# Optimization experiments

Measured on AMD Instinct MI355X. Metric: run time of the kernel, lower is better.

The kernel has to match this reference:

```python
import jax, jax.numpy as jnp
import numpy as np

B, NPTS, T, P, C, D = 2, 32768, 32768, 512, 4, 768


def _sincos_pos_embed(centers, embed_dim):
    # centers: np [P,3]; matches get_3d_sincos_pos_embed
    c = centers - centers.mean(axis=0)
    c = c / np.linalg.norm(c, axis=1).max()
    div = np.exp(np.arange(0, embed_dim, 6) * -(np.log(10000.0) / embed_dim))  # [D/6]
    arg = c[:, None, :] * div[None, :, None]                                   # [P, D/6, 3]
    pe = np.concatenate([np.sin(arg), np.cos(arg)], axis=-1).reshape(centers.shape[0], embed_dim)
    return pe.astype(np.float32)


def setup_inputs() -> dict:
    key = jax.random.key(0)
    ks = jax.random.split(key, 12)
    rng = np.random.default_rng(0)

    # ragged patch sizes (avg 64) summing exactly to T
    sizes = rng.integers(32, 97, size=P).astype(np.int64)
    sizes = np.maximum((sizes * (T / sizes.sum())).astype(np.int64), 1)
    sizes[-1] += T - sizes.sum()
    patch_offset = jnp.asarray(np.concatenate([[0], np.cumsum(sizes)]), dtype=jnp.int32)  # [P+1]

    patch_index = jax.random.randint(ks[0], (T,), 0, NPTS, dtype=jnp.int32)
    latent = jax.random.normal(ks[1], (B, NPTS, C), dtype=jnp.float32)

    s = 0.02
    params = dict(
        w1a=jax.random.normal(ks[2], (C, D), jnp.float32) * s,
        b1a=jnp.zeros((D,), jnp.float32),
        w1b=jax.random.normal(ks[3], (D, D), jnp.float32) * s,
        b1b=jnp.zeros((D,), jnp.float32),
        w2a=jax.random.normal(ks[4], (2 * D, D), jnp.float32) * s,
        b2a=jnp.zeros((D,), jnp.float32),
        g2=jnp.ones((D,), jnp.float32),
        beta2=jnp.zeros((D,), jnp.float32),
        w2b=jax.random.normal(ks[5], (D, D), jnp.float32) * s,
        b2b=jnp.zeros((D,), jnp.float32),
    )

    centers = rng.standard_normal((P, 3))
    pos_embed = jnp.asarray(_sincos_pos_embed(centers, D))[None]  # [1, P, D]

    return dict(latent=latent, patch_index=patch_index, patch_offset=patch_offset,
                pos_embed=pos_embed, **params)


def _ln(x, eps, gamma=None, beta=None):
    mu = x.mean(axis=-1, keepdims=True)
    var = ((x - mu) ** 2).mean(axis=-1, keepdims=True)
    y = (x - mu) * jax.lax.rsqrt(var + eps)
    if gamma is not None:
        y = y * gamma + beta
    return y


def reference(latent, patch_index, patch_offset, pos_embed,
              w1a, b1a, w1b, b1b, w2a, b2a, g2, beta2, w2b, b2b):
    T_ = patch_index.shape[0]
    P_ = patch_offset.shape[0] - 1
    # segment id of each token (repeat_interleave inverse): seg[t] = patch containing t
    seg = jnp.searchsorted(patch_offset[1:], jnp.arange(T_, dtype=patch_offset.dtype), side='right')

    x = latent[:, patch_index, :]                           # [B, T, C] gather
    h = x @ w1a + b1a
    h = jax.nn.gelu(_ln(h, 1e-6), approximate=False)
    h = h @ w1b + b1b                                       # [B, T, D]

    segmax = lambda a: jax.ops.segment_max(a, seg, num_segments=P_)
    y = jax.vmap(segmax)(h)                                 # [B, P, D] ragged max-pool

    h2 = jnp.concatenate([y[:, seg, :], h], axis=-1)        # repeat_interleave + concat
    h2 = h2 @ w2a + b2a
    h2 = jax.nn.gelu(_ln(h2, 1e-5, g2, beta2), approximate=False)
    h2 = h2 @ w2b + b2b                                     # [B, T, D]
    raw_latent = h2

    out = jax.vmap(segmax)(raw_latent) + pos_embed          # [B, P, D]
    return out.astype(raw_latent.dtype), raw_latent
```

## Files before the change

### kernel.cpp

```cpp
#include <hip/hip_runtime.h>
#include <hip/hip_bf16.h>
#include <math.h>

#define B_    2
#define NPTS_ 32768
#define T_    32768
#define P_    512
#define C_    4
#define D_    768
#define M_    (B_ * T_)

typedef __bf16 bf16_t;
typedef __bf16 bf16x8 __attribute__((ext_vector_type(8)));
typedef __bf16 bf16x4 __attribute__((ext_vector_type(4)));
typedef float  f32x4  __attribute__((ext_vector_type(4)));

__device__ inline void gload16(const void* g, void* l) {
  __builtin_amdgcn_global_load_lds(
      (const __attribute__((address_space(1))) void*)g,
      (__attribute__((address_space(3))) void*)l, 16, 0, 0);
}

__device__ inline float gelu_exact(float x) {
  return 0.5f * x * (1.0f + erff(x * 0.70710678118654752f));
}

__device__ inline unsigned fmap(float x) {
  unsigned u = __float_as_uint(x);
  return (u & 0x80000000u) ? ~u : (u | 0x80000000u);
}
__device__ inline float funmap(unsigned u) {
  unsigned v = (u & 0x80000000u) ? (u & 0x7FFFFFFFu) : ~u;
  return __uint_as_float(v);
}

__global__ __launch_bounds__(256) void prep_kernel(
    const int* __restrict__ off, int* __restrict__ seg, uint4* __restrict__ umax,
    const float* __restrict__ w1b, const float* __restrict__ w2a,
    const float* __restrict__ w2b,
    bf16_t* __restrict__ w1bT, bf16_t* __restrict__ w2aTT,
    bf16_t* __restrict__ w2aBT, bf16_t* __restrict__ w2bT) {
  __shared__ float tile[32][33];
  int bid = blockIdx.x, tid = threadIdx.x;
  if (bid < 2304) {
    const float* src; bf16_t* dst;
    int which = bid / 576, r = bid - which * 576;
    if (which == 0)      { src = w1b;             dst = w1bT;  }
    else if (which == 1) { src = w2a;             dst = w2aTT; }
    else if (which == 2) { src = w2a + D_ * D_;   dst = w2aBT; }
    else                 { src = w2b;             dst = w2bT;  }
    int n0 = (r % 24) * 32, k0 = (r / 24) * 32;
    int tx = tid & 31, ty = tid >> 5;
    #pragma unroll
    for (int i = 0; i < 4; ++i)
      tile[ty + 8 * i][tx] = src[(size_t)(k0 + ty + 8 * i) * D_ + n0 + tx];
    __syncthreads();
    #pragma unroll
    for (int i = 0; i < 4; ++i)
      dst[(size_t)(n0 + ty + 8 * i) * D_ + k0 + tx] = (bf16_t)tile[tx][ty + 8 * i];
  } else if (bid < 2432) {
    int t = (bid - 2304) * 256 + tid;
    int lo = 0, hi = P_;
    while (lo < hi) {
      int mid = (lo + hi) >> 1;
      if (off[mid + 1] <= t) lo = mid + 1; else hi = mid;
    }
    seg[t] = lo;
  } else {
    umax[(size_t)(bid - 2432) * 256 + tid] = make_uint4(0, 0, 0, 0);
  }
}

__global__ __launch_bounds__(256) void yconv_kernel(
    const uint4* __restrict__ ymax, bf16_t* __restrict__ y) {
  int t = blockIdx.x * 256 + threadIdx.x;
  uint4 u = ymax[t];
  bf16x4 o;
  o[0] = (bf16_t)funmap(u.x); o[1] = (bf16_t)funmap(u.y);
  o[2] = (bf16_t)funmap(u.z); o[3] = (bf16_t)funmap(u.w);
  *(bf16x4*)(y + (size_t)t * 4) = o;
}

__global__ __launch_bounds__(256) void final2_kernel(
    const uint4* __restrict__ rmax, const float4* __restrict__ pe,
    float4* __restrict__ out) {
  int t = blockIdx.x * 256 + threadIdx.x;
  int row = t / 192, col = t % 192;
  uint4 u = rmax[t];
  float4 p = pe[(row & (P_ - 1)) * 192 + col];
  float4 o;
  o.x = funmap(u.x) + p.x; o.y = funmap(u.y) + p.y;
  o.z = funmap(u.z) + p.z; o.w = funmap(u.w) + p.w;
  out[t] = o;
}

__global__ __launch_bounds__(256) void embed_kernel(
    const float4* __restrict__ latent4, const int* __restrict__ pidx,
    const float* __restrict__ w1a, const float* __restrict__ b1a,
    bf16_t* __restrict__ act1) {
  int wid = threadIdx.x >> 6, lane = threadIdx.x & 63;
  int m = blockIdx.x * 4 + wid;
  int b = m >> 15, t = m & (T_ - 1);
  float4 x = latent4[(size_t)b * NPTS_ + pidx[t]];
  int d8 = lane * 8, d4 = 512 + lane * 4;
  float v[12];
  {
    float4 a0 = *(const float4*)(b1a + d8);
    float4 a1 = *(const float4*)(b1a + d8 + 4);
    float4 a2 = *(const float4*)(b1a + d4);
    v[0]=a0.x; v[1]=a0.y; v[2]=a0.z; v[3]=a0.w;
    v[4]=a1.x; v[5]=a1.y; v[6]=a1.z; v[7]=a1.w;
    v[8]=a2.x; v[9]=a2.y; v[10]=a2.z; v[11]=a2.w;
  }
  float xk[4] = {x.x, x.y, x.z, x.w};
  #pragma unroll
  for (int k = 0; k < 4; ++k) {
    const float* w = w1a + k * D_;
    float4 w0 = *(const float4*)(w + d8);
    float4 w1 = *(const float4*)(w + d8 + 4);
    float4 w2 = *(const float4*)(w + d4);
    float f = xk[k];
    v[0] += f*w0.x; v[1] += f*w0.y; v[2] += f*w0.z; v[3] += f*w0.w;
    v[4] += f*w1.x; v[5] += f*w1.y; v[6] += f*w1.z; v[7] += f*w1.w;
    v[8] += f*w2.x; v[9] += f*w2.y; v[10]+= f*w2.z; v[11]+= f*w2.w;
  }
  float sum = 0.f, sq = 0.f;
  #pragma unroll
  for (int j = 0; j < 12; ++j) { sum += v[j]; sq += v[j]*v[j]; }
  #pragma unroll
  for (int o = 32; o > 0; o >>= 1) { sum += __shfl_xor(sum, o); sq += __shfl_xor(sq, o); }
  float mu = sum * (1.0f / D_);
  float rstd = rsqrtf(sq * (1.0f / D_) - mu * mu + 1e-6f);
  bf16x8 o8; bf16x4 o4;
  #pragma unroll
  for (int j = 0; j < 8; ++j) o8[j] = (bf16_t)gelu_exact((v[j] - mu) * rstd);
  #pragma unroll
  for (int j = 0; j < 4; ++j) o4[j] = (bf16_t)gelu_exact((v[8 + j] - mu) * rstd);
  size_t base = (size_t)m * D_;
  *(bf16x8*)(act1 + base + d8) = o8;
  *(bf16x4*)(act1 + base + d4) = o4;
}

__global__ __launch_bounds__(256) void ln2_kernel(
    const bf16_t* __restrict__ h2pre, const float* __restrict__ z,
    const int* __restrict__ seg, const float* __restrict__ g2,
    const float* __restrict__ beta2, bf16_t* __restrict__ act2) {
  int wid = threadIdx.x >> 6, lane = threadIdx.x & 63;
  int m = blockIdx.x * 4 + wid;
  int b = m >> 15, t = m & (T_ - 1);
  int d8 = lane * 8, d4 = 512 + lane * 4;
  size_t base = (size_t)m * D_;
  const float* zrow = z + (size_t)((b << 9) + seg[t]) * D_;
  bf16x8 i8 = *(const bf16x8*)(h2pre + base + d8);
  bf16x4 i4 = *(const bf16x4*)(h2pre + base + d4);
  float4 z0 = *(const float4*)(zrow + d8);
  float4 z1 = *(const float4*)(zrow + d8 + 4);
  float4 z2 = *(const float4*)(zrow + d4);
  float v[12];
  #pragma unroll
  for (int j = 0; j < 8; ++j) v[j] = (float)i8[j];
  #pragma unroll
  for (int j = 0; j < 4; ++j) v[8 + j] = (float)i4[j];
  v[0]+=z0.x; v[1]+=z0.y; v[2]+=z0.z; v[3]+=z0.w;
  v[4]+=z1.x; v[5]+=z1.y; v[6]+=z1.z; v[7]+=z1.w;
  v[8]+=z2.x; v[9]+=z2.y; v[10]+=z2.z; v[11]+=z2.w;
  float sum = 0.f, sq = 0.f;
  #pragma unroll
  for (int j = 0; j < 12; ++j) { sum += v[j]; sq += v[j]*v[j]; }
  #pragma unroll
  for (int o = 32; o > 0; o >>= 1) { sum += __shfl_xor(sum, o); sq += __shfl_xor(sq, o); }
  float mu = sum * (1.0f / D_);
  float rstd = rsqrtf(sq * (1.0f / D_) - mu * mu + 1e-5f);
  float4 ga = *(const float4*)(g2 + d8);
  float4 gb = *(const float4*)(g2 + d8 + 4);
  float4 gc = *(const float4*)(g2 + d4);
  float4 ba = *(const float4*)(beta2 + d8);
  float4 bb = *(const float4*)(beta2 + d8 + 4);
  float4 bc = *(const float4*)(beta2 + d4);
  float g[12] = {ga.x,ga.y,ga.z,ga.w, gb.x,gb.y,gb.z,gb.w, gc.x,gc.y,gc.z,gc.w};
  float be[12]= {ba.x,ba.y,ba.z,ba.w, bb.x,bb.y,bb.z,bb.w, bc.x,bc.y,bc.z,bc.w};
  bf16x8 o8; bf16x4 o4;
  #pragma unroll
  for (int j = 0; j < 8; ++j) o8[j] = (bf16_t)gelu_exact((v[j] - mu) * rstd * g[j] + be[j]);
  #pragma unroll
  for (int j = 0; j < 4; ++j) o4[j] = (bf16_t)gelu_exact((v[8+j] - mu) * rstd * g[8+j] + be[8+j]);
  *(bf16x8*)(act2 + base + d8) = o8;
  *(bf16x4*)(act2 + base + d4) = o4;
}

#define STAGE_A(P2, KTG)                                                     \
  { _Pragma("unroll")                                                        \
    for (int h = 0; h < 2; ++h) {                                            \
      _Pragma("unroll")                                                      \
      for (int ps = 0; ps < 2; ++ps) {                                       \
        int c = ps * 512 + wid * 64 + lane;                                  \
        int rw = c >> 3;                                                     \
        int cs = (c & 7) ^ (rw & 7);                                         \
        gload16(A + (size_t)(m0 + h * 128 + rw) * 768 + (KTG) + cs * 8,      \
                lds + (P2) * 65536 + h * 16384 + ps * 8192 + wid * 1024);    \
      } } }

#define STAGE_B(P2, KTG)                                                     \
  { _Pragma("unroll")                                                        \
    for (int h = 0; h < 2; ++h) {                                            \
      _Pragma("unroll")                                                      \
      for (int ps = 0; ps < 2; ++ps) {                                       \
        int c = ps * 512 + wid * 64 + lane;                                  \
        int rw = c >> 3;                                                     \
        int cs = (c & 7) ^ (rw & 7);                                         \
        gload16(BT + (size_t)(n0 + h * 128 + rw) * 768 + (KTG) + cs * 8,     \
                lds + (P2) * 65536 + 32768 + h * 16384 + ps * 8192 + wid * 1024); \
      } } }

#define READ_AF0(BASE)                                                       \
  { _Pragma("unroll")                                                        \
    for (int i = 0; i < 4; ++i) {                                            \
      _Pragma("unroll")                                                      \
      for (int s = 0; s < 2; ++s) {                                          \
        int row = i * 16 + lr;                                               \
        int ch = (s * 4 + hi) ^ cx;                                          \
        af0[i][s] = *(const bf16x8*)((BASE) + wm * 16384 + row * 128 + ch * 16); \
      } } }

#define READ_BF0(BASE)                                                       \
  { _Pragma("unroll")                                                        \
    for (int jb = 0; jb < 2; ++jb) {                                         \
      _Pragma("unroll")                                                      \
      for (int s = 0; s < 2; ++s) {                                          \
        int nrow = wn * 64 + jb * 16 + lr;                                   \
        int ch = (s * 4 + hi) ^ cx;                                          \
        bf0[jb][s] = *(const bf16x8*)((BASE) + 32768 + (nrow >> 7) * 16384 + \
                                      (nrow & 127) * 128 + ch * 16);         \
      } } }

template <bool HASBIAS, bool SEGMAX, typename OutT>
__global__ __launch_bounds__(512, 1) void gemm256_kernel(
    const bf16_t* __restrict__ A, const bf16_t* __restrict__ BT,
    const float* __restrict__ bias, OutT* __restrict__ C,
    const int* __restrict__ seg, unsigned* __restrict__ gmax) {
  constexpr int NT = 12;
  __shared__ __align__(16) char lds[131072];
  __shared__ int segm[256];
  int tid = threadIdx.x;
  int wid = tid >> 6, lane = tid & 63;
  int lr = lane & 15, hi = lane >> 4;
  int wm = wid >> 2, wn = wid & 3;

  int gx = gridDim.x;
  int nb = gx * gridDim.y;
  int bid = blockIdx.y * gx + blockIdx.x;
  int w = ((nb & 7) == 0) ? ((bid & 7) * (nb >> 3) + (bid >> 3)) : bid;
  int bx = w % gx, by = w / gx;
  int n0 = bx * 256, m0 = by * 256;

  if (SEGMAX) { if (tid < 256) segm[tid] = seg[(m0 + tid) & (T_ - 1)]; }

  f32x4 acc[8][4] = {};
  bf16x8 af0[4][2], af1[4][2], bf0[2][2], bf1[2][2];
  int cx = lr & 7;

  STAGE_A(0, 0); STAGE_B(0, 0);
  STAGE_A(1, 64); STAGE_B(1, 64);
  asm volatile("s_waitcnt vmcnt(8)" ::: "memory");
  __builtin_amdgcn_s_barrier();
  READ_AF0(lds); READ_BF0(lds);

  for (int j = 0; j < NT; ++j) {
    const char* base  = lds + (j & 1) * 65536;
    const char* baseN = lds + ((j & 1) ^ 1) * 65536;

    #pragma unroll
    for (int i = 0; i < 4; ++i)
      #pragma unroll
      for (int s = 0; s < 2; ++s) {
        int row = 64 + i * 16 + lr;
        int ch = (s * 4 + hi) ^ cx;
        af1[i][s] = *(const bf16x8*)(base + wm * 16384 + row * 128 + ch * 16);
      }
    __builtin_amdgcn_s_setprio(1);
    #pragma unroll
    for (int i = 0; i < 4; ++i)
      #pragma unroll
      for (int jb = 0; jb < 2; ++jb)
        #pragma unroll
        for (int s = 0; s < 2; ++s)
          acc[i][jb] = __builtin_amdgcn_mfma_f32_16x16x32_bf16(af0[i][s], bf0[jb][s], acc[i][jb], 0, 0, 0);
    __builtin_amdgcn_s_setprio(0);
    __builtin_amdgcn_s_barrier();

    #pragma unroll
    for (int jb = 0; jb < 2; ++jb)
      #pragma unroll
      for (int s = 0; s < 2; ++s) {
        int nrow = wn * 64 + 32 + jb * 16 + lr;
        int ch = (s * 4 + hi) ^ cx;
        bf1[jb][s] = *(const bf16x8*)(base + 32768 + (nrow >> 7) * 16384 +
                                      (nrow & 127) * 128 + ch * 16);
      }
    __builtin_amdgcn_s_setprio(1);
    #pragma unroll
    for (int i = 0; i < 4; ++i)
      #pragma unroll
      for (int jb = 0; jb < 2; ++jb)
        #pragma unroll
        for (int s = 0; s < 2; ++s)
          acc[4 + i][jb] = __builtin_amdgcn_mfma_f32_16x16x32_bf16(af1[i][s], bf0[jb][s], acc[4 + i][jb], 0, 0, 0);
    __builtin_amdgcn_s_setprio(0);
    __builtin_amdgcn_s_barrier();

    if (j + 2 < NT) STAGE_A(j & 1, (j + 2) * 64);
    __builtin_amdgcn_s_setprio(1);
    #pragma unroll
    for (int i = 0; i < 4; ++i)
      #pragma unroll
      for (int jb = 0; jb < 2; ++jb)
        #pragma unroll
        for (int s = 0; s < 2; ++s)
          acc[i][2 + jb] = __builtin_amdgcn_mfma_f32_16x16x32_bf16(af0[i][s], bf1[jb][s], acc[i][2 + jb], 0, 0, 0);
    __builtin_amdgcn_s_setprio(0);

    if (j + 1 < NT) {
      if (j + 2 < NT) asm volatile("s_waitcnt vmcnt(4)" ::: "memory");
      else            asm volatile("s_waitcnt vmcnt(0)" ::: "memory");
      __builtin_amdgcn_s_barrier();
      READ_AF0(baseN); READ_BF0(baseN);
      if (j + 2 < NT) STAGE_B(j & 1, (j + 2) * 64);
    }
    __builtin_amdgcn_s_setprio(1);
    #pragma unroll
    for (int i = 0; i < 4; ++i)
      #pragma unroll
      for (int jb = 0; jb < 2; ++jb)
        #pragma unroll
        for (int s = 0; s < 2; ++s)
          acc[4 + i][2 + jb] = __builtin_amdgcn_mfma_f32_16x16x32_bf16(af1[i][s], bf1[jb][s], acc[4 + i][2 + jb], 0, 0, 0);
    __builtin_amdgcn_s_setprio(0);
    __builtin_amdgcn_s_barrier();
  }

  unsigned* smax = reinterpret_cast<unsigned*>(lds);
  int sb = 0, zb = 0;
  if (SEGMAX) {
    sb = segm[0];
    zb = (m0 >> 15) << 9;
    for (int q = tid; q < 16 * 256; q += 512) smax[q] = 0u;
    __syncthreads();
  }

  #pragma unroll
  for (int jn = 0; jn < 4; ++jn) {
    int nl = wn * 64 + jn * 16 + lr;
    int n = n0 + nl;
    float bv = HASBIAS ? bias[n] : 0.f;
    #pragma unroll
    for (int i = 0; i < 8; ++i) {
      int rb = wm * 128 + i * 16 + hi * 4;
      float vv[4];
      #pragma unroll
      for (int r = 0; r < 4; ++r) {
        vv[r] = acc[i][jn][r] + bv;
        C[(size_t)(m0 + rb + r) * 768 + n] = (OutT)vv[r];
      }
      if (SEGMAX) {
        int sA = segm[rb] - sb, sB = segm[rb + 3] - sb;
        if (sA == sB) {
          float mx = fmaxf(fmaxf(vv[0], vv[1]), fmaxf(vv[2], vv[3]));
          atomicMax(&smax[sA * 256 + nl], fmap(mx));
        } else {
          #pragma unroll
          for (int r = 0; r < 4; ++r)
            atomicMax(&smax[(segm[rb + r] - sb) * 256 + nl], fmap(vv[r]));
        }
      }
    }
  }

  if (SEGMAX) {
    __syncthreads();
    int nseg = segm[255] - sb + 1;
    int mlo = m0 & (T_ - 1);
    bool strad_lo = (mlo != 0) && (seg[(mlo - 1)] == sb);
    bool strad_hi = (mlo + 256 < T_) && (seg[(mlo + 256)] == segm[255]);
    for (int q = tid; q < nseg * 256; q += 512) {
      int sl = q >> 8, nl2 = q & 255;
      unsigned val = smax[q];
      unsigned* dst = &gmax[(size_t)(zb + sb + sl) * 768 + n0 + nl2];
      bool bdry = (sl == 0 && strad_lo) || (sl == nseg - 1 && strad_hi);
      if (bdry) atomicMax(dst, val);
      else      *dst = val;
    }
  }
}

extern "C" void kernel_launch(void* const* d_in, const int* in_sizes, int n_in,
                              void* d_out, int out_size, void* d_ws, size_t ws_size,
                              hipStream_t stream) {
  const float* latent       = (const float*)d_in[0];
  const int*   patch_index  = (const int*)d_in[1];
  const int*   patch_offset = (const int*)d_in[2];
  const float* pos_embed    = (const float*)d_in[3];
  const float* w1a  = (const float*)d_in[4];
  const float* b1a  = (const float*)d_in[5];
  const float* w1b  = (const float*)d_in[6];
  const float* b1b  = (const float*)d_in[7];
  const float* w2a  = (const float*)d_in[8];
  const float* b2a  = (const float*)d_in[9];
  const float* g2   = (const float*)d_in[10];
  const float* beta2= (const float*)d_in[11];
  const float* w2b  = (const float*)d_in[12];
  const float* b2b  = (const float*)d_in[13];

  float* out_f   = (float*)d_out;
  float* raw_out = out_f + (size_t)B_ * P_ * D_;

  char* ws = (char*)d_ws;
  size_t off = 0;
  auto take = [&](size_t bytes) {
    off = (off + 255) & ~(size_t)255;
    char* p = ws + off;
    off += bytes;
    return p;
  };
  int*      seg   = (int*)     take((size_t)T_ * 4);
  bf16_t*   w1bT  = (bf16_t*)  take((size_t)D_ * D_ * 2);
  bf16_t*   w2aTT = (bf16_t*)  take((size_t)D_ * D_ * 2);
  bf16_t*   w2aBT = (bf16_t*)  take((size_t)D_ * D_ * 2);
  bf16_t*   w2bT  = (bf16_t*)  take((size_t)D_ * D_ * 2);
  bf16_t*   ybuf  = (bf16_t*)  take((size_t)B_ * P_ * D_ * 2);
  float*    zbuf  = (float*)   take((size_t)B_ * P_ * D_ * 4);
  unsigned* umax  = (unsigned*)take((size_t)2 * B_ * P_ * D_ * 4);
  unsigned* ymax  = umax;
  unsigned* rmax  = umax + (size_t)B_ * P_ * D_;
  bf16_t*   bufY  = (bf16_t*)  take((size_t)M_ * D_ * 2);
  size_t needX = (size_t)M_ * D_ * 2;
  size_t offX  = (off + 255) & ~(size_t)255;
  bf16_t* bufX;
  if (offX + needX <= ws_size) {
    bufX = (bf16_t*)take(needX);
  } else {
    bufX = (bf16_t*)raw_out;
  }

  prep_kernel<<<3968, 256, 0, stream>>>(patch_offset, seg, (uint4*)umax,
                                        w1b, w2a, w2b, w1bT, w2aTT, w2aBT, w2bT);

  embed_kernel<<<M_ / 4, 256, 0, stream>>>((const float4*)latent, patch_index, w1a, b1a, bufX);

  gemm256_kernel<true, true, bf16_t><<<dim3(3, M_/256), 512, 0, stream>>>(
      bufX, w1bT, b1b, bufY, seg, ymax);

  yconv_kernel<<<(B_ * P_ * D_) / (4 * 256), 256, 0, stream>>>((const uint4*)ymax, ybuf);

  gemm256_kernel<true, false, float><<<dim3(3, (B_*P_)/256), 512, 0, stream>>>(
      ybuf, w2aTT, b2a, zbuf, nullptr, nullptr);

  gemm256_kernel<false, false, bf16_t><<<dim3(3, M_/256), 512, 0, stream>>>(
      bufY, w2aBT, nullptr, bufX, nullptr, nullptr);

  ln2_kernel<<<M_ / 4, 256, 0, stream>>>(bufX, zbuf, seg, g2, beta2, bufY);

  gemm256_kernel<true, true, float><<<dim3(3, M_/256), 512, 0, stream>>>(
      bufY, w2bT, b2b, raw_out, seg, rmax);

  final2_kernel<<<(B_ * P_ * D_) / (4 * 256), 256, 0, stream>>>(
      (const uint4*)rmax, (const float4*)pos_embed, (float4*)out_f);
}
```

Before: 438.4 us.

## Merge embed into prep kernel and replace y-conversion plus small GEMM with fp32 zvec

Folds the embedding/LN/GELU pass into the preparation kernel so weight transposes, segment ids, max-buffer clearing and embedding run in one launch, with w1a and bias held in registers across four rows per wave. Drops the bf16 conversion of pooled maxima and the 1024-row bf16 GEMM, computing z directly from the mapped max buffer with a simple fp32 tiled kernel that reads w2a untransposed. This removes two launches and one weight transpose, at the cost of a scalar, non-tensor-core kernel for the small GEMM.

```diff
diff --git a/kernel.cpp b/kernel.cpp
--- a/kernel.cpp
+++ b/kernel.cpp
@@ -34,20 +34,74 @@
   return __uint_as_float(v);
 }
 
-__global__ __launch_bounds__(256) void prep_kernel(
+__global__ __launch_bounds__(256) void bigprep_kernel(
+    const float4* __restrict__ latent4, const int* __restrict__ pidx,
+    const float* __restrict__ w1a, const float* __restrict__ b1a,
+    bf16_t* __restrict__ act1,
     const int* __restrict__ off, int* __restrict__ seg, uint4* __restrict__ umax,
     const float* __restrict__ w1b, const float* __restrict__ w2a,
     const float* __restrict__ w2b,
-    bf16_t* __restrict__ w1bT, bf16_t* __restrict__ w2aTT,
-    bf16_t* __restrict__ w2aBT, bf16_t* __restrict__ w2bT) {
-  __shared__ float tile[32][33];
+    bf16_t* __restrict__ w1bT, bf16_t* __restrict__ w2aBT,
+    bf16_t* __restrict__ w2bT) {
   int bid = blockIdx.x, tid = threadIdx.x;
-  if (bid < 2304) {
+  if (bid < 4096) {
+    int wid = tid >> 6, lane = tid & 63;
+    int mb = bid * 16 + wid * 4;
+    int d8 = lane * 8, d4 = 512 + lane * 4;
+    float bb[12], wreg[4][12];
+    {
+      float4 a0 = *(const float4*)(b1a + d8);
+      float4 a1 = *(const float4*)(b1a + d8 + 4);
+      float4 a2 = *(const float4*)(b1a + d4);
+      bb[0]=a0.x; bb[1]=a0.y; bb[2]=a0.z; bb[3]=a0.w;
+      bb[4]=a1.x; bb[5]=a1.y; bb[6]=a1.z; bb[7]=a1.w;
+      bb[8]=a2.x; bb[9]=a2.y; bb[10]=a2.z; bb[11]=a2.w;
+    }
+    #pragma unroll
+    for (int k = 0; k < 4; ++k) {
+      const float* w = w1a + k * D_;
+      float4 w0 = *(const float4*)(w + d8);
+      float4 w1 = *(const float4*)(w + d8 + 4);
+      float4 w2 = *(const float4*)(w + d4);
+      wreg[k][0]=w0.x; wreg[k][1]=w0.y; wreg[k][2]=w0.z; wreg[k][3]=w0.w;
+      wreg[k][4]=w1.x; wreg[k][5]=w1.y; wreg[k][6]=w1.z; wreg[k][7]=w1.w;
+      wreg[k][8]=w2.x; wreg[k][9]=w2.y; wreg[k][10]=w2.z; wreg[k][11]=w2.w;
+    }
+    for (int rr = 0; rr < 4; ++rr) {
+      int m = mb + rr;
+      int b = m >> 15, t = m & (T_ - 1);
+      float4 x = latent4[(size_t)b * NPTS_ + pidx[t]];
+      float xk[4] = {x.x, x.y, x.z, x.w};
+      float v[12];
+      #pragma unroll
+      for (int j = 0; j < 12; ++j) {
+        v[j] = bb[j];
+        #pragma unroll
+        for (int k = 0; k < 4; ++k) v[j] += xk[k] * wreg[k][j];
+      }
+      float sum = 0.f, sq = 0.f;
+      #pragma unroll
+      for (int j = 0; j < 12; ++j) { sum += v[j]; sq += v[j]*v[j]; }
+      #pragma unroll
+      for (int o = 32; o > 0; o >>= 1) { sum += __shfl_xor(sum, o); sq += __shfl_xor(sq, o); }
+      float mu = sum * (1.0f / D_);
+      float rstd = rsqrtf(sq * (1.0f / D_) - mu * mu + 1e-6f);
+      bf16x8 o8; bf16x4 o4;
+      #pragma unroll
+      for (int j = 0; j < 8; ++j) o8[j] = (bf16_t)gelu_exact((v[j] - mu) * rstd);
+      #pragma unroll
+      for (int j = 0; j < 4; ++j) o4[j] = (bf16_t)gelu_exact((v[8 + j] - mu) * rstd);
+      size_t base = (size_t)m * D_;
+      *(bf16x8*)(act1 + base + d8) = o8;
+      *(bf16x4*)(act1 + base + d4) = o4;
+    }
+  } else if (bid < 5824) {
+    __shared__ float tile[32][33];
+    int r = bid - 4096;
     const float* src; bf16_t* dst;
-    int which = bid / 576, r = bid - which * 576;
+    int which = r / 576; r -= which * 576;
     if (which == 0)      { src = w1b;             dst = w1bT;  }
-    else if (which == 1) { src = w2a;             dst = w2aTT; }
-    else if (which == 2) { src = w2a + D_ * D_;   dst = w2aBT; }
+    else if (which == 1) { src = w2a + D_ * D_;   dst = w2aBT; }
     else                 { src = w2b;             dst = w2bT;  }
     int n0 = (r % 24) * 32, k0 = (r / 24) * 32;
     int tx = tid & 31, ty = tid >> 5;
@@ -58,8 +112,8 @@
     #pragma unroll
     for (int i = 0; i < 4; ++i)
       dst[(size_t)(n0 + ty + 8 * i) * D_ + k0 + tx] = (bf16_t)tile[tx][ty + 8 * i];
-  } else if (bid < 2432) {
-    int t = (bid - 2304) * 256 + tid;
+  } else if (bid < 5952) {
+    int t = (bid - 5824) * 256 + tid;
     int lo = 0, hi = P_;
     while (lo < hi) {
       int mid = (lo + hi) >> 1;
@@ -67,78 +121,37 @@
     }
     seg[t] = lo;
   } else {
-    umax[(size_t)(bid - 2432) * 256 + tid] = make_uint4(0, 0, 0, 0);
-  }
-}
-
-__global__ __launch_bounds__(256) void yconv_kernel(
-    const uint4* __restrict__ ymax, bf16_t* __restrict__ y) {
-  int t = blockIdx.x * 256 + threadIdx.x;
-  uint4 u = ymax[t];
-  bf16x4 o;
-  o[0] = (bf16_t)funmap(u.x); o[1] = (bf16_t)funmap(u.y);
-  o[2] = (bf16_t)funmap(u.z); o[3] = (bf16_t)funmap(u.w);
-  *(bf16x4*)(y + (size_t)t * 4) = o;
-}
-
-__global__ __launch_bounds__(256) void final2_kernel(
-    const uint4* __restrict__ rmax, const float4* __restrict__ pe,
-    float4* __restrict__ out) {
-  int t = blockIdx.x * 256 + threadIdx.x;
-  int row = t / 192, col = t % 192;
-  uint4 u = rmax[t];
-  float4 p = pe[(row & (P_ - 1)) * 192 + col];
-  float4 o;
-  o.x = funmap(u.x) + p.x; o.y = funmap(u.y) + p.y;
-  o.z = funmap(u.z) + p.z; o.w = funmap(u.w) + p.w;
-  out[t] = o;
-}
-
-__global__ __launch_bounds__(256) void embed_kernel(
-    const float4* __restrict__ latent4, const int* __restrict__ pidx,
-    const float* __restrict__ w1a, const float* __restrict__ b1a,
-    bf16_t* __restrict__ act1) {
-  int wid = threadIdx.x >> 6, lane = threadIdx.x & 63;
-  int m = blockIdx.x * 4 + wid;
-  int b = m >> 15, t = m & (T_ - 1);
-  float4 x = latent4[(size_t)b * NPTS_ + pidx[t]];
-  int d8 = lane * 8, d4 = 512 + lane * 4;
-  float v[12];
-  {
-    float4 a0 = *(const float4*)(b1a + d8);
-    float4 a1 = *(const float4*)(b1a + d8 + 4);
-    float4 a2 = *(const float4*)(b1a + d4);
-    v[0]=a0.x; v[1]=a0.y; v[2]=a0.z; v[3]=a0.w;
-    v[4]=a1.x; v[5]=a1.y; v[6]=a1.z; v[7]=a1.w;
-    v[8]=a2.x; v[9]=a2.y; v[10]=a2.z; v[11]=a2.w;
-  }
-  float xk[4] = {x.x, x.y, x.z, x.w};
-  #pragma unroll
-  for (int k = 0; k < 4; ++k) {
-    const float* w = w1a + k * D_;
-    float4 w0 = *(const float4*)(w + d8);
-    float4 w1 = *(const float4*)(w + d8 + 4);
-    float4 w2 = *(const float4*)(w + d4);
-    float f = xk[k];
-    v[0] += f*w0.x; v[1] += f*w0.y; v[2] += f*w0.z; v[3] += f*w0.w;
-    v[4] += f*w1.x; v[5] += f*w1.y; v[6] += f*w1.z; v[7] += f*w1.w;
-    v[8] += f*w2.x; v[9] += f*w2.y; v[10]+= f*w2.z; v[11]+= f*w2.w;
-  }
-  float sum = 0.f, sq = 0.f;
-  #pragma unroll
-  for (int j = 0; j < 12; ++j) { sum += v[j]; sq += v[j]*v[j]; }
-  #pragma unroll
-  for (int o = 32; o > 0; o >>= 1) { sum += __shfl_xor(sum, o); sq += __shfl_xor(sq, o); }
-  float mu = sum * (1.0f / D_);
-  float rstd = rsqrtf(sq * (1.0f / D_) - mu * mu + 1e-6f);
-  bf16x8 o8; bf16x4 o4;
-  #pragma unroll
-  for (int j = 0; j < 8; ++j) o8[j] = (bf16_t)gelu_exact((v[j] - mu) * rstd);
-  #pragma unroll
-  for (int j = 0; j < 4; ++j) o4[j] = (bf16_t)gelu_exact((v[8 + j] - mu) * rstd);
-  size_t base = (size_t)m * D_;
-  *(bf16x8*)(act1 + base + d8) = o8;
-  *(bf16x4*)(act1 + base + d4) = o4;
+    umax[(size_t)(bid - 5952) * 256 + tid] = make_uint4(0, 0, 0, 0);
+  }
+}
+
+__global__ __launch_bounds__(256) void zvec_kernel(
+    const unsigned* __restrict__ ymax, const float* __restrict__ w2a,
+    const float* __restrict__ b2a, float* __restrict__ z) {
+  __shared__ float Aw[32][33], Bw[32][33];
+  int r = blockIdx.x;
+  int m0 = (r / 24) * 32, n0 = (r % 24) * 32;
+  int tx = threadIdx.x & 31, ty = threadIdx.x >> 5;
+  float acc[4] = {0.f, 0.f, 0.f, 0.f};
+  for (int k0 = 0; k0 < D_; k0 += 32) {
+    __syncthreads();
+    #pragma unroll
+    for (int i = 0; i < 4; ++i) {
+      Aw[ty + 8 * i][tx] = funmap(ymax[(size_t)(m0 + ty + 8 * i) * D_ + k0 + tx]);
+      Bw[ty + 8 * i][tx] = w2a[(size_t)(k0 + ty + 8 * i) * D_ + n0 + tx];
+    }
+    __syncthreads();
+    #pragma unroll
+    for (int kk = 0; kk < 32; ++kk) {
+      float bv = Bw[kk][tx];
+      #pragma unroll
+      for (int i = 0; i < 4; ++i) acc[i] += Aw[ty + 8 * i][kk] * bv;
+    }
+  }
+  float bav = b2a[n0 + tx];
+  #pragma unroll
+  for (int i = 0; i < 4; ++i)
+    z[(size_t)(m0 + ty + 8 * i) * D_ + n0 + tx] = acc[i] + bav;
 }
 
 __global__ __launch_bounds__(256) void ln2_kernel(
@@ -175,10 +188,10 @@
   float4 gb = *(const float4*)(g2 + d8 + 4);
   float4 gc = *(const float4*)(g2 + d4);
   float4 ba = *(const float4*)(beta2 + d8);
-  float4 bb = *(const float4*)(beta2 + d8 + 4);
+  float4 bbv = *(const float4*)(beta2 + d8 + 4);
   float4 bc = *(const float4*)(beta2 + d4);
   float g[12] = {ga.x,ga.y,ga.z,ga.w, gb.x,gb.y,gb.z,gb.w, gc.x,gc.y,gc.z,gc.w};
-  float be[12]= {ba.x,ba.y,ba.z,ba.w, bb.x,bb.y,bb.z,bb.w, bc.x,bc.y,bc.z,bc.w};
+  float be[12]= {ba.x,ba.y,ba.z,ba.w, bbv.x,bbv.y,bbv.z,bbv.w, bc.x,bc.y,bc.z,bc.w};
   bf16x8 o8; bf16x4 o4;
   #pragma unroll
   for (int j = 0; j < 8; ++j) o8[j] = (bf16_t)gelu_exact((v[j] - mu) * rstd * g[j] + be[j]);
@@ -186,6 +199,19 @@
   for (int j = 0; j < 4; ++j) o4[j] = (bf16_t)gelu_exact((v[8+j] - mu) * rstd * g[8+j] + be[8+j]);
   *(bf16x8*)(act2 + base + d8) = o8;
   *(bf16x4*)(act2 + base + d4) = o4;
+}
+
+__global__ __launch_bounds__(256) void final2_kernel(
+    const uint4* __restrict__ rmax, const float4* __restrict__ pe,
+    float4* __restrict__ out) {
+  int t = blockIdx.x * 256 + threadIdx.x;
+  int row = t / 192, col = t % 192;
+  uint4 u = rmax[t];
+  float4 p = pe[(row & (P_ - 1)) * 192 + col];
+  float4 o;
+  o.x = funmap(u.x) + p.x; o.y = funmap(u.y) + p.y;
+  o.z = funmap(u.z) + p.z; o.w = funmap(u.w) + p.w;
+  out[t] = o;
 }
 
 #define STAGE_A(P2, KTG)                                                     \
@@ -379,8 +405,8 @@
     __syncthreads();
     int nseg = segm[255] - sb + 1;
     int mlo = m0 & (T_ - 1);
-    bool strad_lo = (mlo != 0) && (seg[(mlo - 1)] == sb);
-    bool strad_hi = (mlo + 256 < T_) && (seg[(mlo + 256)] == segm[255]);
+    bool strad_lo = (mlo != 0) && (seg[mlo - 1] == sb);
+    bool strad_hi = (mlo + 256 < T_) && (seg[mlo + 256] == segm[255]);
     for (int q = tid; q < nseg * 256; q += 512) {
       int sl = q >> 8, nl2 = q & 255;
       unsigned val = smax[q];
@@ -423,10 +449,8 @@
   };
   int*      seg   = (int*)     take((size_t)T_ * 4);
   bf16_t*   w1bT  = (bf16_t*)  take((size_t)D_ * D_ * 2);
-  bf16_t*   w2aTT = (bf16_t*)  take((size_t)D_ * D_ * 2);
   bf16_t*   w2aBT = (bf16_t*)  take((size_t)D_ * D_ * 2);
   bf16_t*   w2bT  = (bf16_t*)  take((size_t)D_ * D_ * 2);
-  bf16_t*   ybuf  = (bf16_t*)  take((size_t)B_ * P_ * D_ * 2);
   float*    zbuf  = (float*)   take((size_t)B_ * P_ * D_ * 4);
   unsigned* umax  = (unsigned*)take((size_t)2 * B_ * P_ * D_ * 4);
   unsigned* ymax  = umax;
@@ -441,18 +465,15 @@
     bufX = (bf16_t*)raw_out;
   }
 
-  prep_kernel<<<3968, 256, 0, stream>>>(patch_offset, seg, (uint4*)umax,
-                                        w1b, w2a, w2b, w1bT, w2aTT, w2aBT, w2bT);
-
-  embed_kernel<<<M_ / 4, 256, 0, stream>>>((const float4*)latent, patch_index, w1a, b1a, bufX);
+  bigprep_kernel<<<7488, 256, 0, stream>>>(
+      (const float4*)latent, patch_index, w1a, b1a, bufX,
+      patch_offset, seg, (uint4*)umax,
+      w1b, w2a, w2b, w1bT, w2aBT, w2bT);
 
   gemm256_kernel<true, true, bf16_t><<<dim3(3, M_/256), 512, 0, stream>>>(
       bufX, w1bT, b1b, bufY, seg, ymax);
 
-  yconv_kernel<<<(B_ * P_ * D_) / (4 * 256), 256, 0, stream>>>((const uint4*)ymax, ybuf);
-
-  gemm256_kernel<true, false, float><<<dim3(3, (B_*P_)/256), 512, 0, stream>>>(
-      ybuf, w2aTT, b2a, zbuf, nullptr, nullptr);
+  zvec_kernel<<<768, 256, 0, stream>>>(ymax, w2a, b2a, zbuf);
 
   gemm256_kernel<false, false, bf16_t><<<dim3(3, M_/256), 512, 0, stream>>>(
       bufY, w2aBT, nullptr, bufX, nullptr, nullptr);
@@ -462,6 +483,6 @@
   gemm256_kernel<true, true, float><<<dim3(3, M_/256), 512, 0, stream>>>(
       bufY, w2bT, b2b, raw_out, seg, rmax);
 
-  final2_kernel<<<(B_ * P_ * D_) / (4 * 256), 256, 0, stream>>>(
+  final2_kernel<<<768, 256, 0, stream>>>(
       (const uint4*)rmax, (const float4*)pos_embed, (float4*)out_f);
 }
```

After: 484.2 us. 1.1x slower.
